# Optimization experiments

Hardware: AMD Instinct MI355X
Metric: run time of the kernel (lower is better)

The kernel has to match this reference:

```python
import jax, jax.numpy as jnp
import numpy as np

B, T, I, H, O = 64, 2048, 128, 256, 128
K1 = 1
K2 = 1


def setup_inputs() -> dict:
    key = jax.random.key(0)
    ks = jax.random.split(key, 8)
    M = H - K1 + 1
    return {
        "x": jax.random.normal(ks[0], (B, T, I), jnp.float32),
        "W_in": jax.random.normal(ks[1], (H, I), jnp.float32) / np.sqrt(I).astype(np.float32),
        "b_in": jax.random.normal(ks[2], (H,), jnp.float32) * 0.01,
        "W_out": jax.random.normal(ks[3], (O, H), jnp.float32) / np.sqrt(H).astype(np.float32),
        "b_out": jax.random.normal(ks[4], (O,), jnp.float32) * 0.01,
        # padded Householder vectors: row i uses its first K+i entries (masked in reference)
        # uniform in [0.5, 1.5] keeps u.u well away from 0 (avoids 2/<u,u> blowup)
        "u_raw": jax.random.uniform(ks[5], (M, H), jnp.float32, 0.5, 1.5),
        "sigmas": jnp.ones((H,), jnp.float32),
        "v_raw": jax.random.uniform(ks[6], (M, H), jnp.float32, 0.5, 1.5),
    }


def _householder_chain(hats):
    # U <- H_last @ ... @ H_0, H_i = I - 2/<u,u> u u^T, applied as rank-1 updates
    Hdim = hats.shape[1]
    def step(Umat, u):
        beta = 2.0 / jnp.dot(u, u)
        return Umat - beta * jnp.outer(u, u @ Umat), None
    U, _ = jax.lax.scan(step, jnp.eye(Hdim, dtype=hats.dtype), hats)
    return U


def reference(x, W_in, b_in, W_out, b_out, u_raw, sigmas, v_raw):
    Hdim = sigmas.shape[0]
    Mu = u_raw.shape[0]
    Mv = v_raw.shape[0]
    # row i of u_hats has entries in cols [0, K1+i), then flipped along cols
    mask_u = jnp.arange(Hdim)[None, :] < (K1 + jnp.arange(Mu))[:, None]
    u_hats = jnp.flip(jnp.where(mask_u, u_raw, 0.0), axis=1)
    mask_v = jnp.arange(Hdim)[None, :] < (K2 + jnp.arange(Mv))[:, None]
    v_hats = jnp.flip(jnp.where(mask_v, v_raw, 0.0), axis=(0, 1))  # torch.flip dims=[0,1]
    U = _householder_chain(u_hats)
    V = _householder_chain(v_hats)
    W = (U * sigmas[None, :]) @ V  # U @ diag(sigmas) @ V
    # precompute input projection for all timesteps: [T, B, H]
    xproj = jnp.einsum('bti,hi->tbh', x, W_in) + b_in
    h0 = jnp.zeros((x.shape[0], Hdim), x.dtype)
    def cell(h, xp):
        h = jnp.tanh(xp + h @ W.T)
        return h, h @ W_out.T + b_out
    _, out = jax.lax.scan(cell, h0, xproj)  # out: [T, B, O]
    return jnp.transpose(out, (1, 0, 2))
```

## Files before the change

### kernel.cpp

```cpp
#include <hip/hip_runtime.h>
#include <hip/hip_bf16.h>
#include <hip/hip_fp16.h>

#define BB 64
#define TT 2048
#define II 128
#define HH 256
#define OO 128
#define RCH 8

typedef _Float16 f16x2 __attribute__((ext_vector_type(2)));
typedef _Float16 f16x8 __attribute__((ext_vector_type(8)));
typedef float f32x4 __attribute__((ext_vector_type(4)));

#if __has_builtin(__builtin_amdgcn_fdot2)
__device__ __forceinline__ float fdot2(f16x2 a, f16x2 b, float c) {
    return __builtin_amdgcn_fdot2(a, b, c, false);
}
#else
__device__ __forceinline__ float fdot2(f16x2 a, f16x2 b, float c) {
    return fmaf((float)a.x, (float)b.x, fmaf((float)a.y, (float)b.y, c));
}
#endif

__device__ __forceinline__ f16x2 u2h(unsigned int u) { return __builtin_bit_cast(f16x2, u); }
__device__ __forceinline__ unsigned int packf16(float a, float b) {
    return __builtin_bit_cast(unsigned int, f16x2{(_Float16)a, (_Float16)b});
}

__device__ __forceinline__ float tanh_fast(float x) {
    float xc = fminf(fmaxf(x, -9.0f), 9.0f);
    float e = __expf(2.0f * xc);
    return (e - 1.0f) * __fdividef(1.0f, e + 1.0f);
}

__device__ __forceinline__ void step_barrier() {
    __builtin_amdgcn_sched_barrier(0);
    asm volatile("s_waitcnt lgkmcnt(0)" ::: "memory");
    __builtin_amdgcn_s_barrier();
    __builtin_amdgcn_sched_barrier(0);
}

__global__ __launch_bounds__(64) void prep_kernel(
    const float* __restrict__ u_raw, const float* __restrict__ v_raw,
    float* __restrict__ u_eff, float* __restrict__ v_eff,
    float* __restrict__ beta_u, float* __restrict__ beta_v)
{
    const int row = blockIdx.x;
    const int lane = threadIdx.x;
    const bool isU = row < HH;
    const int i = isU ? row : row - HH;
    const float* src = isU ? (u_raw + (size_t)i * HH) : (v_raw + (size_t)(HH - 1 - i) * HH);
    float* dst = (isU ? u_eff : v_eff) + (size_t)i * HH;
    const int lo = isU ? (HH - 1 - i) : i;
    float ss = 0.0f;
    for (int c = lane; c < HH; c += 64) {
        float vv = (c >= lo) ? src[HH - 1 - c] : 0.0f;
        dst[c] = vv;
        ss += vv * vv;
    }
    for (int m = 1; m < 64; m <<= 1) ss += __shfl_xor(ss, m, 64);
    if (lane == 0) (isU ? beta_u : beta_v)[i] = 2.0f / ss;
}

__global__ __launch_bounds__(256) void hh_kernel(
    const float* __restrict__ u_eff, const float* __restrict__ v_eff,
    const float* __restrict__ beta_u, const float* __restrict__ beta_v,
    float* __restrict__ Ucol, float* __restrict__ Vrow)
{
    const int wid = blockIdx.x * 4 + (threadIdx.x >> 6);
    const int lane = threadIdx.x & 63;
    const bool isU = wid < HH;
    const int j = isU ? wid : wid - HH;
    const float* eff = isU ? u_eff : v_eff;
    const float* beta = isU ? beta_u : beta_v;

    float cr0 = (j == 4 * lane + 0) ? 1.0f : 0.0f;
    float cr1 = (j == 4 * lane + 1) ? 1.0f : 0.0f;
    float cr2 = (j == 4 * lane + 2) ? 1.0f : 0.0f;
    float cr3 = (j == 4 * lane + 3) ? 1.0f : 0.0f;

    const int i0 = isU ? (HH - 1 - j) : 0;
    for (int i = i0; i < HH; ++i) {
        const float4 v4 = *(const float4*)(eff + (size_t)i * HH + lane * 4);
        float d = v4.x * cr0 + v4.y * cr1 + v4.z * cr2 + v4.w * cr3;
        for (int m = 1; m < 64; m <<= 1) d += __shfl_xor(d, m, 64);
        const float t = beta[i] * d;
        cr0 = fmaf(-t, v4.x, cr0);
        cr1 = fmaf(-t, v4.y, cr1);
        cr2 = fmaf(-t, v4.z, cr2);
        cr3 = fmaf(-t, v4.w, cr3);
    }
    if (isU) {
        *(float4*)(Ucol + (size_t)j * HH + lane * 4) = make_float4(cr0, cr1, cr2, cr3);
    } else {
        Vrow[(size_t)(4 * lane + 0) * HH + j] = cr0;
        Vrow[(size_t)(4 * lane + 1) * HH + j] = cr1;
        Vrow[(size_t)(4 * lane + 2) * HH + j] = cr2;
        Vrow[(size_t)(4 * lane + 3) * HH + j] = cr3;
    }
}

__global__ __launch_bounds__(256) void w_kernel(
    const float* __restrict__ Ucol, const float* __restrict__ Vrow,
    const float* __restrict__ sig, float* __restrict__ Wm)
{
    const int r = blockIdx.x;
    const int c = threadIdx.x;
    float acc = 0.0f;
    #pragma unroll 4
    for (int k = 0; k < HH; ++k) {
        acc = fmaf(Ucol[(size_t)k * HH + r] * sig[k], Vrow[(size_t)k * HH + c], acc);
    }
    Wm[(size_t)r * HH + c] = acc;
}

__device__ __forceinline__ void stage16(_Float16* dst, const float* src) {
    #pragma unroll
    for (int i = 0; i < 4; ++i) {
        float4 f = ((const float4*)src)[i];
        ((f16x2*)dst)[2 * i + 0] = f16x2{(_Float16)f.x, (_Float16)f.y};
        ((f16x2*)dst)[2 * i + 1] = f16x2{(_Float16)f.z, (_Float16)f.w};
    }
}
__device__ __forceinline__ void stage16(_Float16* dst, const __half* src) {
    ((uint4*)dst)[0] = ((const uint4*)src)[0];
    ((uint4*)dst)[1] = ((const uint4*)src)[1];
}
__device__ __forceinline__ void storeC(float* p, float v) { *p = v; }
__device__ __forceinline__ void storeC(__half* p, float v) { *p = __float2half_rn(v); }

template <typename AT, typename OT>
__global__ __launch_bounds__(256) void gemm_mfma(
    const AT* __restrict__ A, const float* __restrict__ Bm,
    const float* __restrict__ bias, OT* __restrict__ C,
    int M, int N, int K)
{
    __shared__ _Float16 As[128][40];
    __shared__ _Float16 Bs[64][40];
    const int tid = threadIdx.x;
    const int m0 = blockIdx.x * 128;
    const int n0 = blockIdx.y * 64;
    const int lane = tid & 63;
    const int w = tid >> 6;
    const int lo = lane & 15;
    const int qd = lane >> 4;
    const int mh = w >> 1;
    const int nh = w & 1;
    const int srow = tid >> 1;
    const int shalf = tid & 1;

    f32x4 acc[4][2] = {};
    for (int k0 = 0; k0 < K; k0 += 32) {
        stage16(&As[srow][shalf * 16], A + (size_t)(m0 + srow) * K + k0 + shalf * 16);
        if (tid < 128)
            stage16(&Bs[srow][shalf * 16], Bm + (size_t)(n0 + srow) * K + k0 + shalf * 16);
        __syncthreads();
        f16x8 af[4], bf[2];
        #pragma unroll
        for (int mt = 0; mt < 4; ++mt)
            af[mt] = *(const f16x8*)&As[64 * mh + 16 * mt + lo][qd * 8];
        #pragma unroll
        for (int nt = 0; nt < 2; ++nt)
            bf[nt] = *(const f16x8*)&Bs[32 * nh + 16 * nt + lo][qd * 8];
        #pragma unroll
        for (int mt = 0; mt < 4; ++mt)
            #pragma unroll
            for (int nt = 0; nt < 2; ++nt)
                acc[mt][nt] = __builtin_amdgcn_mfma_f32_16x16x32_f16(
                    af[mt], bf[nt], acc[mt][nt], 0, 0, 0);
        __syncthreads();
    }
    #pragma unroll
    for (int nt = 0; nt < 2; ++nt) {
        const int n = n0 + 32 * nh + 16 * nt + lo;
        const float bv = bias[n];
        #pragma unroll
        for (int mt = 0; mt < 4; ++mt) {
            const int m = m0 + 64 * mh + 16 * mt + 4 * qd;
            #pragma unroll
            for (int r = 0; r < 4; ++r)
                storeC(C + (size_t)(m + r) * N + n, acc[mt][nt][r] + bv);
        }
    }
}

__global__ __launch_bounds__(512) void recur_kernel(
    const float* __restrict__ Wm,
    const __half* __restrict__ xp,
    __half* __restrict__ hall)
{
    const int b = blockIdx.x;
    const int tid = threadIdx.x;
    const int l = tid & 63;
    const int q = tid >> 6;
    const int lr = l & 31;
    const int hh = l >> 5;

    __shared__ float ps[2][8][HH];

    f16x2 w2[4][16];
    #pragma unroll
    for (int r = 0; r < 4; ++r) {
        const float* Wp = Wm + (size_t)(4 * l + r) * HH + q * 32;
        #pragma unroll
        for (int c4 = 0; c4 < 8; ++c4) {
            float4 f = *(const float4*)(Wp + c4 * 4);
            w2[r][c4 * 2 + 0] = f16x2{(_Float16)f.x, (_Float16)f.y};
            w2[r][c4 * 2 + 1] = f16x2{(_Float16)f.z, (_Float16)f.w};
        }
    }

    const int e = 32 * q + lr;
    const _Float16* xph = (const _Float16*)xp + (size_t)b * TT * HH + e;
    unsigned int* hw = (unsigned int*)(hall + (size_t)b * TT * HH) + (e >> 1);
    const bool st = (l < 32) && !(l & 1);

    _Float16 xpc[RCH], xpn[RCH];
    unsigned int hst[RCH];
    #pragma unroll
    for (int s = 0; s < RCH; ++s) xpc[s] = xph[(size_t)s * HH];

    unsigned int v = 0u;
    int p = 0;
    const int nch = TT / RCH;
    for (int c = 0; c < nch; ++c) {
        if (c + 1 < nch) {
            const _Float16* xn = xph + (size_t)(c + 1) * RCH * HH;
            #pragma unroll
            for (int s = 0; s < RCH; ++s) xpn[s] = xn[(size_t)s * HH];
        }
        #pragma unroll
        for (int s = 0; s < RCH; ++s) {
            float a0 = 0.f, a1 = 0.f, a2 = 0.f, a3 = 0.f;
            #pragma unroll
            for (int j = 0; j < 16; ++j) {
                f16x2 hj = u2h((unsigned int)__builtin_amdgcn_readlane((int)v, 2 * j));
                a0 = fdot2(w2[0][j], hj, a0);
                a1 = fdot2(w2[1][j], hj, a1);
                a2 = fdot2(w2[2][j], hj, a2);
                a3 = fdot2(w2[3][j], hj, a3);
            }
            *(float4*)&ps[p][q][4 * l] = make_float4(a0, a1, a2, a3);
            step_barrier();

            float s4 = (ps[p][4 * hh + 0][e] + ps[p][4 * hh + 1][e])
                     + (ps[p][4 * hh + 2][e] + ps[p][4 * hh + 3][e]);
            float tot = s4 + __shfl_xor(s4, 32, 64);
            float hv = tanh_fast(tot + (float)xpc[s]);
            float ho = __shfl_xor(hv, 1, 64);
            v = packf16(hv, ho);
            hst[s] = v;
            p ^= 1;
        }
        if (st) {
            unsigned int* hwc = hw + (size_t)c * RCH * 128;
            #pragma unroll
            for (int s2 = 0; s2 < RCH; ++s2) hwc[(size_t)s2 * 128] = hst[s2];
        }
        #pragma unroll
        for (int s2 = 0; s2 < RCH; ++s2) xpc[s2] = xpn[s2];
    }
}

extern "C" void kernel_launch(void* const* d_in, const int* in_sizes, int n_in,
                              void* d_out, int out_size, void* d_ws, size_t ws_size,
                              hipStream_t stream) {
    const float* x     = (const float*)d_in[0];
    const float* W_in  = (const float*)d_in[1];
    const float* b_in  = (const float*)d_in[2];
    const float* W_out = (const float*)d_in[3];
    const float* b_out = (const float*)d_in[4];
    const float* u_raw = (const float*)d_in[5];
    const float* sig   = (const float*)d_in[6];
    const float* v_raw = (const float*)d_in[7];
    float* out = (float*)d_out;

    char* ws = (char*)d_ws;
    size_t off = 0;
    auto alloc = [&](size_t bytes) -> void* {
        void* p = (void*)(ws + off);
        off += (bytes + 255) & ~((size_t)255);
        return p;
    };
    float* u_eff  = (float*)alloc((size_t)HH * HH * 4);
    float* v_eff  = (float*)alloc((size_t)HH * HH * 4);
    float* beta_u = (float*)alloc((size_t)HH * 4);
    float* beta_v = (float*)alloc((size_t)HH * 4);
    float* Ucol   = (float*)alloc((size_t)HH * HH * 4);
    float* Vrow   = (float*)alloc((size_t)HH * HH * 4);
    float* Wm     = (float*)alloc((size_t)HH * HH * 4);
    __half* xpbuf = (__half*)alloc((size_t)BB * TT * HH * 2);
    __half* hall  = (__half*)alloc((size_t)BB * TT * HH * 2);
    (void)ws_size; (void)in_sizes; (void)n_in; (void)out_size;

    prep_kernel<<<2 * HH, 64, 0, stream>>>(u_raw, v_raw, u_eff, v_eff, beta_u, beta_v);
    hh_kernel<<<(2 * HH) / 4, 256, 0, stream>>>(u_eff, v_eff, beta_u, beta_v, Ucol, Vrow);
    w_kernel<<<HH, HH, 0, stream>>>(Ucol, Vrow, sig, Wm);
    gemm_mfma<float, __half>
        <<<dim3((BB * TT) / 128, HH / 64), 256, 0, stream>>>(x, W_in, b_in, xpbuf, BB * TT, HH, II);
    recur_kernel<<<BB, 512, 0, stream>>>(Wm, xpbuf, hall);
    gemm_mfma<__half, float>
        <<<dim3((BB * TT) / 128, OO / 64), 256, 0, stream>>>(hall, W_out, b_out, out, BB * TT, OO, HH);
}
```

Before: 1.572 ms.

## Halve recurrence block size and broadcast hidden state through shared memory

The recurrent kernel now runs with 4 waves instead of 8. Each wave covers 64 input columns of W and reads the previous hidden state from a small shared-memory vector with vector loads, replacing cross-lane readlane broadcasts and the shuffle-based reduction and packing. Each thread now owns one hidden element, so the partial-sum reduction is a plain 4-way add with no shuffles, and it writes its own fp16 output. The aim is to shorten the per-timestep dependency chain and make the per-step barrier cheaper. The cost is twice the fdot2 work and twice the weight registers per thread.

```diff
diff --git a/kernel.cpp b/kernel.cpp
--- a/kernel.cpp
+++ b/kernel.cpp
@@ -185,7 +185,7 @@
     }
 }
 
-__global__ __launch_bounds__(512) void recur_kernel(
+__global__ __launch_bounds__(256, 1) void recur_kernel(
     const float* __restrict__ Wm,
     const __half* __restrict__ xp,
     __half* __restrict__ hall)
@@ -194,70 +194,81 @@
     const int tid = threadIdx.x;
     const int l = tid & 63;
     const int q = tid >> 6;
-    const int lr = l & 31;
-    const int hh = l >> 5;
-
-    __shared__ float ps[2][8][HH];
-
-    f16x2 w2[4][16];
+
+    __shared__ float ps[2][4][HH];
+    __shared__ __align__(16) _Float16 hx[HH];
+
+    f16x2 w2[4][32];
     #pragma unroll
     for (int r = 0; r < 4; ++r) {
-        const float* Wp = Wm + (size_t)(4 * l + r) * HH + q * 32;
-        #pragma unroll
-        for (int c4 = 0; c4 < 8; ++c4) {
-            float4 f = *(const float4*)(Wp + c4 * 4);
-            w2[r][c4 * 2 + 0] = f16x2{(_Float16)f.x, (_Float16)f.y};
-            w2[r][c4 * 2 + 1] = f16x2{(_Float16)f.z, (_Float16)f.w};
+        const float* Wp = Wm + (size_t)(4 * l + r) * HH + 64 * q;
+        #pragma unroll
+        for (int c4 = 0; c4 < 16; ++c4) {
+            float4 f = *(const float4*)(Wp + 4 * c4);
+            w2[r][2 * c4 + 0] = f16x2{(_Float16)f.x, (_Float16)f.y};
+            w2[r][2 * c4 + 1] = f16x2{(_Float16)f.z, (_Float16)f.w};
         }
     }
-
-    const int e = 32 * q + lr;
-    const _Float16* xph = (const _Float16*)xp + (size_t)b * TT * HH + e;
-    unsigned int* hw = (unsigned int*)(hall + (size_t)b * TT * HH) + (e >> 1);
-    const bool st = (l < 32) && !(l & 1);
-
-    _Float16 xpc[RCH], xpn[RCH];
-    unsigned int hst[RCH];
+    if (tid < HH / 2) ((unsigned int*)hx)[tid] = 0u;
+    __syncthreads();
+
+    const _Float16* xpw = (const _Float16*)xp + (size_t)b * TT * HH + tid;
+    unsigned short* hw = (unsigned short*)hall + (size_t)b * TT * HH + tid;
+
+    _Float16 xpc[RCH], xpn[RCH], hst[RCH];
     #pragma unroll
-    for (int s = 0; s < RCH; ++s) xpc[s] = xph[(size_t)s * HH];
-
-    unsigned int v = 0u;
-    int p = 0;
+    for (int s = 0; s < RCH; ++s) xpc[s] = xpw[(size_t)s * HH];
+
     const int nch = TT / RCH;
     for (int c = 0; c < nch; ++c) {
         if (c + 1 < nch) {
-            const _Float16* xn = xph + (size_t)(c + 1) * RCH * HH;
+            const _Float16* xn = xpw + (size_t)(c + 1) * RCH * HH;
             #pragma unroll
             for (int s = 0; s < RCH; ++s) xpn[s] = xn[(size_t)s * HH];
         }
         #pragma unroll
         for (int s = 0; s < RCH; ++s) {
+            const int p = s & 1;
+            const uint4* hbp = (const uint4*)&hx[64 * q];
+            uint4 hb[8];
+            #pragma unroll
+            for (int g = 0; g < 8; ++g) hb[g] = hbp[g];
             float a0 = 0.f, a1 = 0.f, a2 = 0.f, a3 = 0.f;
             #pragma unroll
-            for (int j = 0; j < 16; ++j) {
-                f16x2 hj = u2h((unsigned int)__builtin_amdgcn_readlane((int)v, 2 * j));
-                a0 = fdot2(w2[0][j], hj, a0);
-                a1 = fdot2(w2[1][j], hj, a1);
-                a2 = fdot2(w2[2][j], hj, a2);
-                a3 = fdot2(w2[3][j], hj, a3);
+            for (int g = 0; g < 8; ++g) {
+                f16x2 p0 = u2h(hb[g].x), p1 = u2h(hb[g].y);
+                f16x2 p2 = u2h(hb[g].z), p3 = u2h(hb[g].w);
+                a0 = fdot2(w2[0][4 * g + 0], p0, a0);
+                a1 = fdot2(w2[1][4 * g + 0], p0, a1);
+                a2 = fdot2(w2[2][4 * g + 0], p0, a2);
+                a3 = fdot2(w2[3][4 * g + 0], p0, a3);
+                a0 = fdot2(w2[0][4 * g + 1], p1, a0);
+                a1 = fdot2(w2[1][4 * g + 1], p1, a1);
+                a2 = fdot2(w2[2][4 * g + 1], p1, a2);
+                a3 = fdot2(w2[3][4 * g + 1], p1, a3);
+                a0 = fdot2(w2[0][4 * g + 2], p2, a0);
+                a1 = fdot2(w2[1][4 * g + 2], p2, a1);
+                a2 = fdot2(w2[2][4 * g + 2], p2, a2);
+                a3 = fdot2(w2[3][4 * g + 2], p2, a3);
+                a0 = fdot2(w2[0][4 * g + 3], p3, a0);
+                a1 = fdot2(w2[1][4 * g + 3], p3, a1);
+                a2 = fdot2(w2[2][4 * g + 3], p3, a2);
+                a3 = fdot2(w2[3][4 * g + 3], p3, a3);
             }
             *(float4*)&ps[p][q][4 * l] = make_float4(a0, a1, a2, a3);
             step_barrier();
 
-            float s4 = (ps[p][4 * hh + 0][e] + ps[p][4 * hh + 1][e])
-                     + (ps[p][4 * hh + 2][e] + ps[p][4 * hh + 3][e]);
-            float tot = s4 + __shfl_xor(s4, 32, 64);
-            float hv = tanh_fast(tot + (float)xpc[s]);
-            float ho = __shfl_xor(hv, 1, 64);
-            v = packf16(hv, ho);
-            hst[s] = v;
-            p ^= 1;
+            float sum = (ps[p][0][tid] + ps[p][1][tid])
+                      + (ps[p][2][tid] + ps[p][3][tid]);
+            float h = tanh_fast(sum + (float)xpc[s]);
+            _Float16 hh = (_Float16)h;
+            hx[tid] = hh;
+            hst[s] = hh;
         }
-        if (st) {
-            unsigned int* hwc = hw + (size_t)c * RCH * 128;
-            #pragma unroll
-            for (int s2 = 0; s2 < RCH; ++s2) hwc[(size_t)s2 * 128] = hst[s2];
-        }
+        unsigned short* hwc = hw + (size_t)c * RCH * HH;
+        #pragma unroll
+        for (int s2 = 0; s2 < RCH; ++s2)
+            hwc[(size_t)s2 * HH] = __builtin_bit_cast(unsigned short, hst[s2]);
         #pragma unroll
         for (int s2 = 0; s2 < RCH; ++s2) xpc[s2] = xpn[s2];
     }
@@ -299,7 +310,7 @@
     w_kernel<<<HH, HH, 0, stream>>>(Ucol, Vrow, sig, Wm);
     gemm_mfma<float, __half>
         <<<dim3((BB * TT) / 128, HH / 64), 256, 0, stream>>>(x, W_in, b_in, xpbuf, BB * TT, HH, II);
-    recur_kernel<<<BB, 512, 0, stream>>>(Wm, xpbuf, hall);
+    recur_kernel<<<BB, 256, 0, stream>>>(Wm, xpbuf, hall);
     gemm_mfma<__half, float>
         <<<dim3((BB * TT) / 128, OO / 64), 256, 0, stream>>>(hall, W_out, b_out, out, BB * TT, OO, HH);
 }
```

After: 1.384 ms. 12.0% less time.
